# Kernel optimization log

Hardware: AMD Instinct MI355X
Metric: run time of the kernel (lower is better)

## Reference

```python
import jax, jax.numpy as jnp
import numpy as np

T, B, N = 256, 128, 64
START_IDX, END_IDX = 1, 2  # Offsets.GO, Offsets.EOS
NEG = -10000.0


def setup_inputs() -> dict:
    key = jax.random.key(0)
    k1, k2, k3 = jax.random.split(key, 3)
    unary = jax.random.normal(k1, (T, B, N), dtype=jnp.float32)          # [T, B, N] emissions
    trans = jax.random.normal(k2, (1, N, N), dtype=jnp.float32) * 0.1    # [1, N_to, N_from]
    lengths = jax.random.randint(k3, (B,), 1, T + 1)                      # 1 <= len <= T
    return {"unary": unary, "trans": trans, "lengths": lengths}


def _crf_log_partition(unary, trans, lengths):
    # unary: [T, B, N], trans: [1, N, N], lengths: [B] -> [B] log Z
    batch_size, n_tags = unary.shape[1], unary.shape[2]
    alphas0 = jnp.full((batch_size, 1, n_tags), NEG, dtype=unary.dtype)
    alphas0 = alphas0.at[:, 0, START_IDX].set(0.0)

    def step(alphas, xi):
        unary_t, i = xi  # unary_t: [B, N], i: scalar timestep
        # scores[b, to, fr] = alphas[b, 0, fr] + trans[0, to, fr] + unary_t[b, to]
        scores = alphas + trans + unary_t[:, :, None]            # [B, N, N]
        new_alphas = jax.nn.logsumexp(scores, axis=2)[:, None, :]  # [B, 1, N]
        # keep new alphas while the sequence is still active (i < length),
        # otherwise carry the old alphas forward (matches masked_fill logic).
        alphas = jnp.where((i < lengths)[:, None, None], new_alphas, alphas)
        return alphas, None

    steps = jnp.arange(unary.shape[0])
    alphas, _ = jax.lax.scan(step, alphas0, (unary, steps))
    terminal = alphas + trans[:, END_IDX]                         # [B, 1, N]
    return jax.nn.logsumexp(terminal, axis=2).squeeze(1)          # [B]


def reference(unary, trans, lengths):
    return _crf_log_partition(unary, trans, lengths)
```

## Files before the change

### kernel.cpp

```cpp
#include <hip/hip_runtime.h>

#define T_STEPS 256
#define B_SIZE  128
#define N_TAGS  64
#define BN_     8192
#define SEGS    16
#define SEGL    16
#define START_IDX 1
#define END_IDX 2

typedef float  f32x4  __attribute__((ext_vector_type(4)));
typedef float  f32x2  __attribute__((ext_vector_type(2)));
typedef short  bf16x8 __attribute__((ext_vector_type(8)));

union U8 { unsigned u[4]; bf16x8 v; };
union F4 { f32x4 v; f32x2 h[2]; float f[4]; };

__device__ __forceinline__ float fexp2(float x){float r;asm("v_exp_f32 %0, %1":"=v"(r):"v"(x));return r;}
__device__ __forceinline__ float flog2(float x){float r;asm("v_log_f32 %0, %1":"=v"(r):"v"(x));return r;}
__device__ __forceinline__ float frcp(float x){float r;asm("v_rcp_f32 %0, %1":"=v"(r):"v"(x));return r;}
__device__ __forceinline__ unsigned cvtpk(float lo,float hi){unsigned r;asm("v_cvt_pk_bf16_f32 %0, %1, %2":"=v"(r):"v"(lo),"v"(hi));return r;}
__device__ __forceinline__ void swap32(unsigned &a, unsigned &b){asm("v_permlane32_swap_b32 %0, %1":"+v"(a),"+v"(b));}
__device__ __forceinline__ void swap16(unsigned &a, unsigned &b){asm("v_permlane16_swap_b32 %0, %1":"+v"(a),"+v"(b));}
__device__ __forceinline__ f32x2 pkmul(f32x2 a, f32x2 b){f32x2 r;asm("v_pk_mul_f32 %0, %1, %2":"=v"(r):"v"(a),"v"(b));return r;}

#define MFMA16(A, B, C) __builtin_amdgcn_mfma_f32_16x16x32_bf16(A, B, C, 0, 0, 0)

__device__ __forceinline__ void wait24(){ asm volatile("s_waitcnt vmcnt(24)" ::: "memory"); __builtin_amdgcn_sched_barrier(0); }
__device__ __forceinline__ void wait16(){ asm volatile("s_waitcnt vmcnt(16)" ::: "memory"); __builtin_amdgcn_sched_barrier(0); }
__device__ __forceinline__ void wait8 (){ asm volatile("s_waitcnt vmcnt(8)"  ::: "memory"); __builtin_amdgcn_sched_barrier(0); }
__device__ __forceinline__ void wait0 (){ asm volatile("s_waitcnt vmcnt(0)"  ::: "memory"); __builtin_amdgcn_sched_barrier(0); }
__device__ __forceinline__ void wait28(){ asm volatile("s_waitcnt vmcnt(28)" ::: "memory"); __builtin_amdgcn_sched_barrier(0); }

#define IDP() do { _Pragma("unroll") \
  for (int c=0;c<2;++c) { _Pragma("unroll") \
    for (int cc=0;cc<4;++cc) { _Pragma("unroll") \
      for (int m=0;m<4;++m) { \
        int k0 = 32*c + 8*g + 2*m, n = 16*cc + col; \
        unsigned lo = (k0==n)?0x3F80u:0u, hi=(k0+1==n)?0x3F80u:0u; \
        P[c][cc].u[m] = lo | (hi<<16); } } } } while(0)

#define EVG() do { _Pragma("unroll") \
  for (int tt=0;tt<4;++tt) { _Pragma("unroll") \
    for (int r=0;r<4;++r) ev[tt][r] = __shfl(eul, 16*tt + 4*g + r, 64); } } while(0)

#define EVSCALE() do { _Pragma("unroll") \
  for (int tt=0;tt<4;++tt) { f32x2 e01,e23; \
    e01[0]=ev[tt][0]; e01[1]=ev[tt][1]; e23[0]=ev[tt][2]; e23[1]=ev[tt][3]; \
    _Pragma("unroll") for (int cc=0;cc<4;++cc) { \
      Dt[tt][cc].h[0]=pkmul(Dt[tt][cc].h[0],e01); \
      Dt[tt][cc].h[1]=pkmul(Dt[tt][cc].h[1],e23); } } } while(0)

#define RESCC() do { C += 44.361419555836498f; \
  f32x2 iv; iv[0]=5.421010862427522e-20f; iv[1]=5.421010862427522e-20f; \
  _Pragma("unroll") for (int tt=0;tt<4;++tt) { _Pragma("unroll") for (int cc=0;cc<4;++cc) { \
    Dt[tt][cc].h[0]=pkmul(Dt[tt][cc].h[0],iv); Dt[tt][cc].h[1]=pkmul(Dt[tt][cc].h[1],iv); } } } while(0)

#define CVTP() do { _Pragma("unroll") \
  for (int cc=0;cc<4;++cc) { \
    unsigned p00 = cvtpk(Dt[0][cc].f[0], Dt[0][cc].f[1]); \
    unsigned p01 = cvtpk(Dt[0][cc].f[2], Dt[0][cc].f[3]); \
    unsigned p10 = cvtpk(Dt[1][cc].f[0], Dt[1][cc].f[1]); \
    unsigned p11 = cvtpk(Dt[1][cc].f[2], Dt[1][cc].f[3]); \
    unsigned p20 = cvtpk(Dt[2][cc].f[0], Dt[2][cc].f[1]); \
    unsigned p21 = cvtpk(Dt[2][cc].f[2], Dt[2][cc].f[3]); \
    unsigned p30 = cvtpk(Dt[3][cc].f[0], Dt[3][cc].f[1]); \
    unsigned p31 = cvtpk(Dt[3][cc].f[2], Dt[3][cc].f[3]); \
    swap32(p00, p10); swap32(p01, p11); swap32(p20, p30); swap32(p21, p31); \
    swap16(p00, p10); swap16(p01, p11); swap16(p20, p30); swap16(p21, p31); \
    P[0][cc].u[0]=p00; P[0][cc].u[1]=p01; P[0][cc].u[2]=p10; P[0][cc].u[3]=p11; \
    P[1][cc].u[0]=p20; P[1][cc].u[1]=p21; P[1][cc].u[2]=p30; P[1][cc].u[3]=p31; } } while(0)

#define MFMAB() do { _Pragma("unroll") \
  for (int cc=0;cc<4;++cc) { _Pragma("unroll") \
    for (int tt=0;tt<4;++tt) { \
      f32x4 acc = MFMA16(EA[tt][0].v, P[0][cc].v, zf); \
      Dt[tt][cc].v = MFMA16(EA[tt][1].v, P[1][cc].v, acc); } } } while(0)

#define STOREP(DST) do { _Pragma("unroll") \
  for (int cc=0;cc<4;++cc) { _Pragma("unroll") \
    for (int c=0;c<2;++c) { \
      uint4 q; q.x=P[c][cc].u[0]; q.y=P[c][cc].u[1]; q.z=P[c][cc].u[2]; q.w=P[c][cc].u[3]; \
      *(uint4*)((DST) + (cc*2+c)*256) = q; } } } while(0)

__global__ __launch_bounds__(64, 2)
void crf_seg_kernel(const float* __restrict__ u, const float* __restrict__ trans,
                    const int* __restrict__ lengths,
                    unsigned* __restrict__ Mout, float* __restrict__ Cout) {
    const int bid  = blockIdx.x;
    const int b    = bid & (B_SIZE - 1);
    const int s    = bid >> 7;
    const int lane = threadIdx.x;
    const int col  = lane & 15;
    const int g    = lane >> 4;
    const float K = 1.4426950408889634f;
    const f32x4 zf = {0.f, 0.f, 0.f, 0.f};

    const int len = lengths[b];
    int n_act = len - 1 - s*SEGL;
    n_act = max(0, min(SEGL, n_act));
    unsigned* dst = Mout + (size_t)(b*SEGS + s) * 2048 + lane * 4;

    U8 P[2][4];
    if (n_act == 0) {
        IDP();
        STOREP(dst);
        if (lane == 0) Cout[b*SEGS + s] = 0.0f;
        return;
    }

    __shared__ float sT[64 * 65];
    {
#pragma unroll
        for (int k = 0; k < 64; ++k) sT[k*65 + lane] = trans[k*64 + lane];
    }
    __syncthreads();

    const bool front = (s < 8);
    U8 EA[4][2];
    if (!front) {
#pragma unroll
        for (int tt = 0; tt < 4; ++tt) {
#pragma unroll
            for (int c = 0; c < 2; ++c) {
                const float* p = &sT[(16*tt + col)*65 + 32*c + 8*g];
#pragma unroll
                for (int j2 = 0; j2 < 4; ++j2)
                    EA[tt][c].u[j2] = cvtpk(fexp2(p[2*j2]*K), fexp2(p[2*j2+1]*K));
            }
        }
    } else {
#pragma unroll
        for (int tt = 0; tt < 4; ++tt) {
#pragma unroll
            for (int c = 0; c < 2; ++c) {
#pragma unroll
                for (int j2 = 0; j2 < 4; ++j2) {
                    const int a0i = 32*c + 8*g + 2*j2;
                    EA[tt][c].u[j2] = cvtpk(fexp2(sT[a0i*65 + 16*tt + col] * K),
                                            fexp2(sT[(a0i+1)*65 + 16*tt + col] * K));
                }
            }
        }
    }

    const float* ub = u + (size_t)b * 64 + lane;
    float Ur[16];
    if (!front) {
        const int t0 = 16*s + 1;
#pragma unroll
        for (int i = 0; i < 16; ++i) Ur[i] = ub[(size_t)min(t0 + i, T_STEPS - 1) * BN_];
    } else {
        const int th = 16*s + n_act;
#pragma unroll
        for (int i = 0; i < 16; ++i) Ur[i] = ub[(size_t)max(th - i, 0) * BN_];
    }

    float C = 0.0f;
    float ev[4][4];
    F4 Dt[4][4];
    { float eul = fexp2(Ur[0] * K); EVG(); }

    if (!front) {
        IDP();
#pragma unroll 16
        for (int i = 0; i < 16; ++i) {
            if (i >= n_act) break;
            MFMAB();
            EVSCALE();
            if (i == 7) RESCC();
            CVTP();
            if (i < 15) { float eul = fexp2(Ur[i+1] * K); EVG(); }
        }
    } else {
#pragma unroll
        for (int tt = 0; tt < 4; ++tt) {
#pragma unroll
            for (int cc = 0; cc < 4; ++cc) {
#pragma unroll
                for (int r = 0; r < 4; ++r)
                    Dt[tt][cc].f[r] = (tt == cc && 4*g + r == col) ? 1.0f : 0.0f;
            }
        }
#pragma unroll 16
        for (int i = 0; i < 16; ++i) {
            if (i >= n_act) break;
            EVSCALE();
            if (i == 7) RESCC();
            CVTP();
            MFMAB();
            if (i < 15) { float eul = fexp2(Ur[i+1] * K); EVG(); }
        }
        CVTP();
    }

    STOREP(dst);
    if (lane == 0) Cout[b*SEGS + s] = C;
}

#define MLOAD(SL, SEG) do { \
    const unsigned* _mp = mbase + (size_t)(SEG) * 2048; \
    const unsigned* _mq = _mp + 1024; \
    asm volatile("global_load_dwordx4 %0, %1, off"             : "=v"(SL[0].v) : "v"(_mp)); \
    asm volatile("global_load_dwordx4 %0, %1, off offset:1024" : "=v"(SL[1].v) : "v"(_mp)); \
    asm volatile("global_load_dwordx4 %0, %1, off offset:2048" : "=v"(SL[2].v) : "v"(_mp)); \
    asm volatile("global_load_dwordx4 %0, %1, off offset:3072" : "=v"(SL[3].v) : "v"(_mp)); \
    asm volatile("global_load_dwordx4 %0, %1, off"             : "=v"(SL[4].v) : "v"(_mq)); \
    asm volatile("global_load_dwordx4 %0, %1, off offset:1024" : "=v"(SL[5].v) : "v"(_mq)); \
    asm volatile("global_load_dwordx4 %0, %1, off offset:2048" : "=v"(SL[6].v) : "v"(_mq)); \
    asm volatile("global_load_dwordx4 %0, %1, off offset:3072" : "=v"(SL[7].v) : "v"(_mq)); \
} while (0)

#define PSTEP(WN, SL, LD) do { \
    wait##WN(); \
    U8 Af0, Af1; \
    { float vs = (g < 2) ? a0 : a1; \
      float f0=__shfl(vs,sbase+0,64), f1=__shfl(vs,sbase+1,64); \
      float f2=__shfl(vs,sbase+2,64), f3=__shfl(vs,sbase+3,64); \
      float f4=__shfl(vs,sbase+4,64), f5=__shfl(vs,sbase+5,64); \
      float f6=__shfl(vs,sbase+6,64), f7=__shfl(vs,sbase+7,64); \
      Af0.u[0]=cvtpk(f0,f1); Af0.u[1]=cvtpk(f2,f3); Af0.u[2]=cvtpk(f4,f5); Af0.u[3]=cvtpk(f6,f7); } \
    { float vs = (g < 2) ? a2 : a3; \
      float f0=__shfl(vs,sbase+0,64), f1=__shfl(vs,sbase+1,64); \
      float f2=__shfl(vs,sbase+2,64), f3=__shfl(vs,sbase+3,64); \
      float f4=__shfl(vs,sbase+4,64), f5=__shfl(vs,sbase+5,64); \
      float f6=__shfl(vs,sbase+6,64), f7=__shfl(vs,sbase+7,64); \
      Af1.u[0]=cvtpk(f0,f1); Af1.u[1]=cvtpk(f2,f3); Af1.u[2]=cvtpk(f4,f5); Af1.u[3]=cvtpk(f6,f7); } \
    f32x4 q0 = MFMA16(Af0.v, SL[0].v, zf); q0 = MFMA16(Af1.v, SL[1].v, q0); \
    f32x4 q1 = MFMA16(Af0.v, SL[2].v, zf); q1 = MFMA16(Af1.v, SL[3].v, q1); \
    f32x4 q2 = MFMA16(Af0.v, SL[4].v, zf); q2 = MFMA16(Af1.v, SL[5].v, q2); \
    f32x4 q3 = MFMA16(Af0.v, SL[6].v, zf); q3 = MFMA16(Af1.v, SL[7].v, q3); \
    float n0 = q0[0], n1 = q1[0], n2 = q2[0], n3 = q3[0]; \
    float mm = fmaxf(fmaxf(n0, n1), fmaxf(n2, n3)); \
    mm = fmaxf(mm, __shfl_xor(mm, 1, 64)); mm = fmaxf(mm, __shfl_xor(mm, 2, 64)); \
    mm = fmaxf(mm, __shfl_xor(mm, 4, 64)); mm = fmaxf(mm, __shfl_xor(mm, 8, 64)); \
    float inv = frcp(mm); C2 += LN2 * flog2(mm); \
    a0 = n0 * inv; a1 = n1 * inv; a2 = n2 * inv; a3 = n3 * inv; \
    if ((LD) >= 0) { MLOAD(SL, LD); } \
} while (0)

__global__ __launch_bounds__(128, 1)
void crf_comb_kernel(const float* __restrict__ u, const float* __restrict__ trans,
                     const unsigned* __restrict__ Mbuf, const float* __restrict__ Cseg,
                     float* __restrict__ out) {
    const int tid  = threadIdx.x;
    const int wid  = tid >> 6;
    const int lane = tid & 63;
    const int col  = lane & 15;
    const int g    = lane >> 4;
    const int b    = blockIdx.x;
    const float K = 1.4426950408889634f, LN2 = 0.6931471805599453f;
    const f32x4 zf = {0.f, 0.f, 0.f, 0.f};

    __shared__ float sX[64], sY[64], sC[2];

    float a0, a1, a2, a3;
    if (wid == 0) {
        a0 = fexp2((u[(size_t)b*64 +  0 + col] + trans[( 0 + col)*64 + START_IDX]) * K);
        a1 = fexp2((u[(size_t)b*64 + 16 + col] + trans[(16 + col)*64 + START_IDX]) * K);
        a2 = fexp2((u[(size_t)b*64 + 32 + col] + trans[(32 + col)*64 + START_IDX]) * K);
        a3 = fexp2((u[(size_t)b*64 + 48 + col] + trans[(48 + col)*64 + START_IDX]) * K);
    } else {
        a0 = fexp2(trans[END_IDX*64 +  0 + col] * K);
        a1 = fexp2(trans[END_IDX*64 + 16 + col] * K);
        a2 = fexp2(trans[END_IDX*64 + 32 + col] * K);
        a3 = fexp2(trans[END_IDX*64 + 48 + col] * K);
    }

    const int sbase = (lane & 48) | ((g & 1) << 3);
    const unsigned* mbase = Mbuf + (size_t)b * SEGS * 2048 + lane * 4;

    U8 MP0[8], MP1[8], MP2[8], MP3[8];
    float C2 = 0.0f;

    if (wid == 0) {
        MLOAD(MP0, 0); MLOAD(MP1, 1); MLOAD(MP2, 2); MLOAD(MP3, 3);
        PSTEP(24, MP0,  4); PSTEP(24, MP1,  5); PSTEP(24, MP2,  6); PSTEP(24, MP3,  7);
        PSTEP(24, MP0, -1); PSTEP(16, MP1, -1); PSTEP(8,  MP2, -1); PSTEP(0,  MP3, -1);
    } else {
        MLOAD(MP0, 15); MLOAD(MP1, 14); MLOAD(MP2, 13); MLOAD(MP3, 12);
        PSTEP(24, MP0, 11); PSTEP(24, MP1, 10); PSTEP(24, MP2,  9); PSTEP(24, MP3,  8);
        PSTEP(24, MP0, -1); PSTEP(16, MP1, -1); PSTEP(8,  MP2, -1); PSTEP(0,  MP3, -1);
    }

    if (g == 0) {
        float* dstv = wid ? sY : sX;
        dstv[ 0 + col] = a0; dstv[16 + col] = a1;
        dstv[32 + col] = a2; dstv[48 + col] = a3;
    }
    if (wid == 1) {
        float cs = (lane < SEGS) ? Cseg[b*SEGS + lane] : 0.0f;
#pragma unroll
        for (int m = 1; m < 64; m <<= 1) cs += __shfl_xor(cs, m, 64);
        if (lane == 0) sC[1] = C2 + cs;
    } else if (lane == 0) sC[0] = C2;
    __syncthreads();

    if (tid < 16) {
        float part = 0.0f;
#pragma unroll
        for (int cc = 0; cc < 4; ++cc)
            part = fmaf(sX[16*cc + tid], sY[16*cc + tid], part);
        part += __shfl_xor(part, 1, 64);
        part += __shfl_xor(part, 2, 64);
        part += __shfl_xor(part, 4, 64);
        part += __shfl_xor(part, 8, 64);
        if (tid == 0) out[b] = sC[0] + sC[1] + LN2 * flog2(part);
    }
}

#define LOAD4O(RB, PTR) do { const float* _p = (PTR); \
    asm volatile("global_load_dwordx4 %0, %1, off"            : "=v"(RB[0].v) : "v"(_p)); \
    asm volatile("global_load_dwordx4 %0, %1, off offset:64"  : "=v"(RB[1].v) : "v"(_p)); \
    asm volatile("global_load_dwordx4 %0, %1, off offset:128" : "=v"(RB[2].v) : "v"(_p)); \
    asm volatile("global_load_dwordx4 %0, %1, off offset:192" : "=v"(RB[3].v) : "v"(_p)); \
} while (0)

template<bool RS, bool SNAPW>
__device__ __forceinline__ void stepfn(F4 (&D)[4], F4 (&UB)[4], const U8 (&A)[4][2],
                                       bool ccw, F4 (&wS)[4], float &snapC, float &C) {
    const float K = 1.4426950408889634f, LN2 = 0.6931471805599453f;
    const f32x4 zf = {0.f, 0.f, 0.f, 0.f};
    F4 W[4];
#pragma unroll
    for (int tt = 0; tt < 4; ++tt) {
#pragma unroll
        for (int r = 0; r < 4; ++r) W[tt].f[r] = D[tt].f[r] * fexp2(UB[tt].f[r] * K);
    }
    if (RS) {
        float m0 = fmaxf(fmaxf(W[0].f[0], W[0].f[1]), fmaxf(W[0].f[2], W[0].f[3]));
        float m1 = fmaxf(fmaxf(W[1].f[0], W[1].f[1]), fmaxf(W[1].f[2], W[1].f[3]));
        float m2 = fmaxf(fmaxf(W[2].f[0], W[2].f[1]), fmaxf(W[2].f[2], W[2].f[3]));
        float m3 = fmaxf(fmaxf(W[3].f[0], W[3].f[1]), fmaxf(W[3].f[2], W[3].f[3]));
        float mm = fmaxf(fmaxf(m0, m1), fmaxf(m2, m3));
        mm = fmaxf(mm, __shfl_xor(mm, 16, 64));
        mm = fmaxf(mm, __shfl_xor(mm, 32, 64));
        float inv = frcp(mm);
        C += LN2 * flog2(mm);
        f32x2 iv; iv[0] = inv; iv[1] = inv;
#pragma unroll
        for (int tt = 0; tt < 4; ++tt) {
            W[tt].h[0] = pkmul(W[tt].h[0], iv);
            W[tt].h[1] = pkmul(W[tt].h[1], iv);
        }
    }
    if (SNAPW) {
        if (__ballot(ccw)) {
#pragma unroll
            for (int tt = 0; tt < 4; ++tt) {
#pragma unroll
                for (int r = 0; r < 4; ++r)
                    wS[tt].f[r] = ccw ? W[tt].f[r] : wS[tt].f[r];
            }
            snapC = ccw ? C : snapC;
        }
    }
    unsigned p00 = cvtpk(W[0].f[0], W[0].f[1]), p01 = cvtpk(W[0].f[2], W[0].f[3]);
    unsigned p10 = cvtpk(W[1].f[0], W[1].f[1]), p11 = cvtpk(W[1].f[2], W[1].f[3]);
    unsigned p20 = cvtpk(W[2].f[0], W[2].f[1]), p21 = cvtpk(W[2].f[2], W[2].f[3]);
    unsigned p30 = cvtpk(W[3].f[0], W[3].f[1]), p31 = cvtpk(W[3].f[2], W[3].f[3]);
    swap32(p00, p10); swap32(p01, p11); swap32(p20, p30); swap32(p21, p31);
    swap16(p00, p10); swap16(p01, p11); swap16(p20, p30); swap16(p21, p31);
    U8 b0, b1;
    b0.u[0] = p00; b0.u[1] = p01; b0.u[2] = p10; b0.u[3] = p11;
    b1.u[0] = p20; b1.u[1] = p21; b1.u[2] = p30; b1.u[3] = p31;
#pragma unroll
    for (int tt = 0; tt < 4; ++tt) {
        f32x4 acc = MFMA16(A[tt][0].v, b0.v, zf);
        D[tt].v   = MFMA16(A[tt][1].v, b1.v, acc);
    }
}

__device__ __forceinline__ void make_frags(const float* sT, int wid, int col, int g,
                                           U8 (&A)[4][2], F4 (&D)[4]) {
    const float K = 1.4426950408889634f;
    if (wid == 0) {
#pragma unroll
        for (int tt = 0; tt < 4; ++tt) {
#pragma unroll
            for (int c = 0; c < 2; ++c) {
                const float* p = &sT[(16*tt + col)*64 + 32*c + 8*g];
#pragma unroll
                for (int j2 = 0; j2 < 4; ++j2)
                    A[tt][c].u[j2] = cvtpk(fexp2(p[2*j2]*K), fexp2(p[2*j2+1]*K));
            }
        }
#pragma unroll
        for (int tt = 0; tt < 4; ++tt) {
#pragma unroll
            for (int r = 0; r < 4; ++r)
                D[tt].f[r] = fexp2(sT[(16*tt + 4*g + r)*64 + START_IDX] * K);
        }
    } else {
#pragma unroll
        for (int tt = 0; tt < 4; ++tt) {
#pragma unroll
            for (int c = 0; c < 2; ++c) {
#pragma unroll
                for (int j2 = 0; j2 < 4; ++j2) {
                    const int a0 = 32*c + 8*g + 2*j2;
                    A[tt][c].u[j2] = cvtpk(fexp2(sT[a0*64 + 16*tt + col] * K),
                                           fexp2(sT[(a0+1)*64 + 16*tt + col] * K));
                }
            }
        }
#pragma unroll
        for (int tt = 0; tt < 4; ++tt) {
#pragma unroll
            for (int r = 0; r < 4; ++r)
                D[tt].f[r] = fexp2(sT[END_IDX*64 + 16*tt + 4*g + r] * K);
        }
    }
}

__launch_bounds__(128, 1)
__global__ void crf_fb_old(const float* __restrict__ src,
                           const float* __restrict__ trans,
                           const int* __restrict__ lengths,
                           float* __restrict__ out) {
    const int tid  = threadIdx.x;
    const int wid  = tid >> 6;
    const int lane = tid & 63;
    const int col  = lane & 15;
    const int g    = lane >> 4;
    const int bidx = blockIdx.x * 16 + col;

    __shared__ __align__(16) float sT[N_TAGS * N_TAGS];
    __shared__ __align__(16) float sW[N_TAGS * 16];
    __shared__ __align__(16) float sV[N_TAGS * 16];
    __shared__ float sCf[16], sCb[16];

    {
        const float4* t4 = (const float4*)trans;
        float4* s4 = (float4*)sT;
#pragma unroll
        for (int k2 = 0; k2 < 8; ++k2) s4[k2 * 128 + tid] = t4[k2 * 128 + tid];
    }
    __syncthreads();

    const float LN2 = 0.6931471805599453f;
    const int len = lengths[bidx];
    const int M   = (len - 1) >> 1;
    const int Kb  = (len - 1) - M;

    U8 A[4][2];
    F4 D[4];
    make_frags(sT, wid, col, g, A, D);

    int need = (wid == 0) ? (M + 1) : Kb;
    int mx = need;
#pragma unroll
    for (int m = 1; m < 64; m <<= 1) mx = max(mx, __shfl_xor(mx, m, 64));
    mx = __builtin_amdgcn_readfirstlane(mx);

    const int base = bidx * 64 + 4 * g;
    float C = 0.0f, snapC = 0.0f;
    F4 wS[4];
#pragma unroll
    for (int tt = 0; tt < 4; ++tt) wS[tt] = D[tt];

    F4 R0[4], R1[4], R2[4], R3[4], R4_[4], R5[4], R6[4], R7[4];

    if (wid == 0) {
        const float* pf = src + base;
        LOAD4O(R0, pf);            LOAD4O(R1, pf + BN_);
        LOAD4O(R2, pf + 2*BN_);    LOAD4O(R3, pf + 3*BN_);
        LOAD4O(R4_, pf + 4*BN_);   LOAD4O(R5, pf + 5*BN_);
        LOAD4O(R6, pf + 6*BN_);    LOAD4O(R7, pf + 7*BN_);
        const float* pn = pf + 8 * BN_;
        const int Nf = (mx + 7) & ~7;
        for (int s = 0; s < Nf; s += 8) {
#define FSTEP(QQ, RB, RSF) do { \
            const int t_ = s + (QQ); \
            wait28(); \
            stepfn<RSF, true>(D, RB, A, (t_ == M), wS, snapC, C); \
            LOAD4O(RB, pn); pn += BN_; \
        } while (0)
            FSTEP(0, R0, false); FSTEP(1, R1, false); FSTEP(2, R2, false);
            FSTEP(3, R3, false); FSTEP(4, R4_, false); FSTEP(5, R5, false);
            FSTEP(6, R6, false); FSTEP(7, R7, true);
#undef FSTEP
        }
        wait0();
    } else {
        const float* pb = src + base;
        {
#define PRIME(RB, q) do { int tq = max(len - 1 - (q), 0); LOAD4O(RB, pb + tq * BN_); } while (0)
            PRIME(R0, 0); PRIME(R1, 1); PRIME(R2, 2); PRIME(R3, 3);
            PRIME(R4_, 4); PRIME(R5, 5); PRIME(R6, 6); PRIME(R7, 7);
#undef PRIME
        }
        int tP = len - 9;
        const int Nb = (mx + 7) & ~7;
        for (int s = 0; s < Nb; s += 8) {
#define BSTEP(QQ, RB, RSF) do { \
            const int k_ = s + (QQ) + 1; \
            wait28(); \
            stepfn<RSF, false>(D, RB, A, false, wS, snapC, C); \
            if (__ballot(k_ == Kb)) { \
                const bool cc = (k_ == Kb); \
                _Pragma("unroll") \
                for (int tt = 0; tt < 4; ++tt) { \
                    _Pragma("unroll") \
                    for (int r = 0; r < 4; ++r) \
                        wS[tt].f[r] = cc ? D[tt].f[r] : wS[tt].f[r]; \
                } \
                snapC = cc ? C : snapC; \
            } \
            int tc = max(tP, 0); LOAD4O(RB, pb + tc * BN_); tP -= 1; \
        } while (0)
            BSTEP(0, R0, false); BSTEP(1, R1, false); BSTEP(2, R2, false);
            BSTEP(3, R3, false); BSTEP(4, R4_, false); BSTEP(5, R5, false);
            BSTEP(6, R6, false); BSTEP(7, R7, true);
#undef BSTEP
        }
        wait0();
    }

    {
        float* dstv = (wid == 0) ? sW : sV;
#pragma unroll
        for (int tt = 0; tt < 4; ++tt) {
#pragma unroll
            for (int r = 0; r < 4; ++r)
                dstv[(16*tt + 4*g + r) * 16 + col] = wS[tt].f[r];
        }
        if (g == 0) { if (wid == 0) sCf[col] = snapC; else sCb[col] = snapC; }
    }
    __syncthreads();
    if (wid == 0) {
        float part = 0.0f;
#pragma unroll
        for (int j = 0; j < 16; ++j) {
            const int n = g * 16 + j;
            part = fmaf(sW[n * 16 + col], sV[n * 16 + col], part);
        }
        part += __shfl_xor(part, 16, 64);
        part += __shfl_xor(part, 32, 64);
        if (g == 0) out[bidx] = sCf[col] + sCb[col] + LN2 * flog2(part);
    }
}

extern "C" void kernel_launch(void* const* d_in, const int* in_sizes, int n_in,
                              void* d_out, int out_size, void* d_ws, size_t ws_size,
                              hipStream_t stream) {
    const float* unary   = (const float*)d_in[0];
    const float* trans   = (const float*)d_in[1];
    const int*   lengths = (const int*)d_in[2];
    float* out = (float*)d_out;

    const size_t mcount = (size_t)B_SIZE * SEGS * 2048;
    const size_t need   = mcount * 4 + (size_t)B_SIZE * SEGS * 4;
    if (ws_size >= need) {
        unsigned* Mbuf = (unsigned*)d_ws;
        float* Cseg = (float*)((unsigned*)d_ws + mcount);
        hipLaunchKernelGGL(crf_seg_kernel, dim3(B_SIZE * SEGS), dim3(64), 0, stream,
                           unary, trans, lengths, Mbuf, Cseg);
        hipLaunchKernelGGL(crf_comb_kernel, dim3(B_SIZE), dim3(128), 0, stream,
                           unary, trans, Mbuf, Cseg, out);
    } else {
        hipLaunchKernelGGL(crf_fb_old, dim3(B_SIZE / 16), dim3(128), 0, stream,
                           unary, trans, lengths, out);
    }
}
```

Before: 33.37 us.

## Fuse segment and combine kernels using atomic last-block-done counter

Merges the per-segment transfer-matrix kernel and the combine kernel into one launch. Each 128-thread block now computes two segments (one front, one back) for a batch row, and the last of the 8 blocks per row, found through an atomic counter, performs the combine step. This removes the second kernel launch and the gap between the two kernels. In exchange it adds a hipMemsetAsync per call, a threadfence/atomic handshake, and shared-memory setup for the larger block, which may lower occupancy.

```diff
diff --git a/kernel.cpp b/kernel.cpp
--- a/kernel.cpp
+++ b/kernel.cpp
@@ -82,121 +82,6 @@
     for (int c=0;c<2;++c) { \
       uint4 q; q.x=P[c][cc].u[0]; q.y=P[c][cc].u[1]; q.z=P[c][cc].u[2]; q.w=P[c][cc].u[3]; \
       *(uint4*)((DST) + (cc*2+c)*256) = q; } } } while(0)
-
-__global__ __launch_bounds__(64, 2)
-void crf_seg_kernel(const float* __restrict__ u, const float* __restrict__ trans,
-                    const int* __restrict__ lengths,
-                    unsigned* __restrict__ Mout, float* __restrict__ Cout) {
-    const int bid  = blockIdx.x;
-    const int b    = bid & (B_SIZE - 1);
-    const int s    = bid >> 7;
-    const int lane = threadIdx.x;
-    const int col  = lane & 15;
-    const int g    = lane >> 4;
-    const float K = 1.4426950408889634f;
-    const f32x4 zf = {0.f, 0.f, 0.f, 0.f};
-
-    const int len = lengths[b];
-    int n_act = len - 1 - s*SEGL;
-    n_act = max(0, min(SEGL, n_act));
-    unsigned* dst = Mout + (size_t)(b*SEGS + s) * 2048 + lane * 4;
-
-    U8 P[2][4];
-    if (n_act == 0) {
-        IDP();
-        STOREP(dst);
-        if (lane == 0) Cout[b*SEGS + s] = 0.0f;
-        return;
-    }
-
-    __shared__ float sT[64 * 65];
-    {
-#pragma unroll
-        for (int k = 0; k < 64; ++k) sT[k*65 + lane] = trans[k*64 + lane];
-    }
-    __syncthreads();
-
-    const bool front = (s < 8);
-    U8 EA[4][2];
-    if (!front) {
-#pragma unroll
-        for (int tt = 0; tt < 4; ++tt) {
-#pragma unroll
-            for (int c = 0; c < 2; ++c) {
-                const float* p = &sT[(16*tt + col)*65 + 32*c + 8*g];
-#pragma unroll
-                for (int j2 = 0; j2 < 4; ++j2)
-                    EA[tt][c].u[j2] = cvtpk(fexp2(p[2*j2]*K), fexp2(p[2*j2+1]*K));
-            }
-        }
-    } else {
-#pragma unroll
-        for (int tt = 0; tt < 4; ++tt) {
-#pragma unroll
-            for (int c = 0; c < 2; ++c) {
-#pragma unroll
-                for (int j2 = 0; j2 < 4; ++j2) {
-                    const int a0i = 32*c + 8*g + 2*j2;
-                    EA[tt][c].u[j2] = cvtpk(fexp2(sT[a0i*65 + 16*tt + col] * K),
-                                            fexp2(sT[(a0i+1)*65 + 16*tt + col] * K));
-                }
-            }
-        }
-    }
-
-    const float* ub = u + (size_t)b * 64 + lane;
-    float Ur[16];
-    if (!front) {
-        const int t0 = 16*s + 1;
-#pragma unroll
-        for (int i = 0; i < 16; ++i) Ur[i] = ub[(size_t)min(t0 + i, T_STEPS - 1) * BN_];
-    } else {
-        const int th = 16*s + n_act;
-#pragma unroll
-        for (int i = 0; i < 16; ++i) Ur[i] = ub[(size_t)max(th - i, 0) * BN_];
-    }
-
-    float C = 0.0f;
-    float ev[4][4];
-    F4 Dt[4][4];
-    { float eul = fexp2(Ur[0] * K); EVG(); }
-
-    if (!front) {
-        IDP();
-#pragma unroll 16
-        for (int i = 0; i < 16; ++i) {
-            if (i >= n_act) break;
-            MFMAB();
-            EVSCALE();
-            if (i == 7) RESCC();
-            CVTP();
-            if (i < 15) { float eul = fexp2(Ur[i+1] * K); EVG(); }
-        }
-    } else {
-#pragma unroll
-        for (int tt = 0; tt < 4; ++tt) {
-#pragma unroll
-            for (int cc = 0; cc < 4; ++cc) {
-#pragma unroll
-                for (int r = 0; r < 4; ++r)
-                    Dt[tt][cc].f[r] = (tt == cc && 4*g + r == col) ? 1.0f : 0.0f;
-            }
-        }
-#pragma unroll 16
-        for (int i = 0; i < 16; ++i) {
-            if (i >= n_act) break;
-            EVSCALE();
-            if (i == 7) RESCC();
-            CVTP();
-            MFMAB();
-            if (i < 15) { float eul = fexp2(Ur[i+1] * K); EVG(); }
-        }
-        CVTP();
-    }
-
-    STOREP(dst);
-    if (lane == 0) Cout[b*SEGS + s] = C;
-}
 
 #define MLOAD(SL, SEG) do { \
     const unsigned* _mp = mbase + (size_t)(SEG) * 2048; \
@@ -239,61 +124,183 @@
     if ((LD) >= 0) { MLOAD(SL, LD); } \
 } while (0)
 
-__global__ __launch_bounds__(128, 1)
-void crf_comb_kernel(const float* __restrict__ u, const float* __restrict__ trans,
-                     const unsigned* __restrict__ Mbuf, const float* __restrict__ Cseg,
-                     float* __restrict__ out) {
+__global__ __launch_bounds__(128, 2)
+void crf_one(const float* __restrict__ u, const float* __restrict__ trans,
+             const int* __restrict__ lengths, unsigned* __restrict__ Mbuf,
+             float* __restrict__ Cseg, unsigned* __restrict__ cnt,
+             float* __restrict__ out) {
     const int tid  = threadIdx.x;
     const int wid  = tid >> 6;
     const int lane = tid & 63;
     const int col  = lane & 15;
     const int g    = lane >> 4;
-    const int b    = blockIdx.x;
+    const int bid  = blockIdx.x;
+    const int b    = bid & (B_SIZE - 1);
+    const int p    = bid >> 7;
     const float K = 1.4426950408889634f, LN2 = 0.6931471805599453f;
     const f32x4 zf = {0.f, 0.f, 0.f, 0.f};
 
+    __shared__ float sT[64 * 65];
     __shared__ float sX[64], sY[64], sC[2];
-
-    float a0, a1, a2, a3;
-    if (wid == 0) {
-        a0 = fexp2((u[(size_t)b*64 +  0 + col] + trans[( 0 + col)*64 + START_IDX]) * K);
-        a1 = fexp2((u[(size_t)b*64 + 16 + col] + trans[(16 + col)*64 + START_IDX]) * K);
-        a2 = fexp2((u[(size_t)b*64 + 32 + col] + trans[(32 + col)*64 + START_IDX]) * K);
-        a3 = fexp2((u[(size_t)b*64 + 48 + col] + trans[(48 + col)*64 + START_IDX]) * K);
-    } else {
-        a0 = fexp2(trans[END_IDX*64 +  0 + col] * K);
-        a1 = fexp2(trans[END_IDX*64 + 16 + col] * K);
-        a2 = fexp2(trans[END_IDX*64 + 32 + col] * K);
-        a3 = fexp2(trans[END_IDX*64 + 48 + col] * K);
-    }
-
-    const int sbase = (lane & 48) | ((g & 1) << 3);
-    const unsigned* mbase = Mbuf + (size_t)b * SEGS * 2048 + lane * 4;
-
-    U8 MP0[8], MP1[8], MP2[8], MP3[8];
-    float C2 = 0.0f;
-
-    if (wid == 0) {
-        MLOAD(MP0, 0); MLOAD(MP1, 1); MLOAD(MP2, 2); MLOAD(MP3, 3);
-        PSTEP(24, MP0,  4); PSTEP(24, MP1,  5); PSTEP(24, MP2,  6); PSTEP(24, MP3,  7);
-        PSTEP(24, MP0, -1); PSTEP(16, MP1, -1); PSTEP(8,  MP2, -1); PSTEP(0,  MP3, -1);
-    } else {
-        MLOAD(MP0, 15); MLOAD(MP1, 14); MLOAD(MP2, 13); MLOAD(MP3, 12);
-        PSTEP(24, MP0, 11); PSTEP(24, MP1, 10); PSTEP(24, MP2,  9); PSTEP(24, MP3,  8);
-        PSTEP(24, MP0, -1); PSTEP(16, MP1, -1); PSTEP(8,  MP2, -1); PSTEP(0,  MP3, -1);
-    }
-
-    if (g == 0) {
-        float* dstv = wid ? sY : sX;
-        dstv[ 0 + col] = a0; dstv[16 + col] = a1;
-        dstv[32 + col] = a2; dstv[48 + col] = a3;
-    }
-    if (wid == 1) {
-        float cs = (lane < SEGS) ? Cseg[b*SEGS + lane] : 0.0f;
-#pragma unroll
-        for (int m = 1; m < 64; m <<= 1) cs += __shfl_xor(cs, m, 64);
-        if (lane == 0) sC[1] = C2 + cs;
-    } else if (lane == 0) sC[0] = C2;
+    __shared__ int  sRet;
+
+    {
+#pragma unroll
+        for (int k = 0; k < 32; ++k) {
+            const int row = 2*k + wid;
+            sT[row*65 + lane] = trans[row*64 + lane];
+        }
+    }
+    __syncthreads();
+
+    const int len = lengths[b];
+    const int s   = (wid == 0) ? p : (8 + p);
+    const bool front = (wid == 0);
+    int n_act = len - 1 - s*SEGL;
+    n_act = max(0, min(SEGL, n_act));
+    unsigned* dst = Mbuf + (size_t)(b*SEGS + s) * 2048 + lane * 4;
+
+    {
+        U8 P[2][4];
+        float C = 0.0f;
+
+        if (n_act == 0) {
+            IDP();
+        } else {
+            U8 EA[4][2];
+            if (!front) {
+#pragma unroll
+                for (int tt = 0; tt < 4; ++tt) {
+#pragma unroll
+                    for (int c = 0; c < 2; ++c) {
+                        const float* pp = &sT[(16*tt + col)*65 + 32*c + 8*g];
+#pragma unroll
+                        for (int j2 = 0; j2 < 4; ++j2)
+                            EA[tt][c].u[j2] = cvtpk(fexp2(pp[2*j2]*K), fexp2(pp[2*j2+1]*K));
+                    }
+                }
+            } else {
+#pragma unroll
+                for (int tt = 0; tt < 4; ++tt) {
+#pragma unroll
+                    for (int c = 0; c < 2; ++c) {
+#pragma unroll
+                        for (int j2 = 0; j2 < 4; ++j2) {
+                            const int a0i = 32*c + 8*g + 2*j2;
+                            EA[tt][c].u[j2] = cvtpk(fexp2(sT[a0i*65 + 16*tt + col] * K),
+                                                    fexp2(sT[(a0i+1)*65 + 16*tt + col] * K));
+                        }
+                    }
+                }
+            }
+
+            const float* ub = u + (size_t)b * 64 + lane;
+            float Ur[16];
+            if (!front) {
+                const int t0 = 16*s + 1;
+#pragma unroll
+                for (int i = 0; i < 16; ++i) Ur[i] = ub[(size_t)min(t0 + i, T_STEPS - 1) * BN_];
+            } else {
+                const int th = 16*s + n_act;
+#pragma unroll
+                for (int i = 0; i < 16; ++i) Ur[i] = ub[(size_t)max(th - i, 0) * BN_];
+            }
+
+            float ev[4][4];
+            F4 Dt[4][4];
+            { float eul = fexp2(Ur[0] * K); EVG(); }
+
+            if (!front) {
+                IDP();
+#pragma unroll 16
+                for (int i = 0; i < 16; ++i) {
+                    if (i >= n_act) break;
+                    MFMAB();
+                    EVSCALE();
+                    if (i == 7) RESCC();
+                    CVTP();
+                    if (i < 15) { float eul = fexp2(Ur[i+1] * K); EVG(); }
+                }
+            } else {
+#pragma unroll
+                for (int tt = 0; tt < 4; ++tt) {
+#pragma unroll
+                    for (int cc = 0; cc < 4; ++cc) {
+#pragma unroll
+                        for (int r = 0; r < 4; ++r)
+                            Dt[tt][cc].f[r] = (tt == cc && 4*g + r == col) ? 1.0f : 0.0f;
+                    }
+                }
+#pragma unroll 16
+                for (int i = 0; i < 16; ++i) {
+                    if (i >= n_act) break;
+                    EVSCALE();
+                    if (i == 7) RESCC();
+                    CVTP();
+                    MFMAB();
+                    if (i < 15) { float eul = fexp2(Ur[i+1] * K); EVG(); }
+                }
+                CVTP();
+            }
+        }
+
+        STOREP(dst);
+        if (lane == 0) Cseg[b*SEGS + s] = C;
+    }
+
+    __syncthreads();
+    if (tid == 0) {
+        __threadfence();
+        unsigned old = atomicAdd(&cnt[b], 1u);
+        sRet = (old == 7u) ? 1 : 0;
+    }
+    __syncthreads();
+    if (!sRet) return;
+
+    __threadfence();
+
+    {
+        float a0, a1, a2, a3;
+        if (wid == 0) {
+            a0 = fexp2((u[(size_t)b*64 +  0 + col] + trans[( 0 + col)*64 + START_IDX]) * K);
+            a1 = fexp2((u[(size_t)b*64 + 16 + col] + trans[(16 + col)*64 + START_IDX]) * K);
+            a2 = fexp2((u[(size_t)b*64 + 32 + col] + trans[(32 + col)*64 + START_IDX]) * K);
+            a3 = fexp2((u[(size_t)b*64 + 48 + col] + trans[(48 + col)*64 + START_IDX]) * K);
+        } else {
+            a0 = fexp2(trans[END_IDX*64 +  0 + col] * K);
+            a1 = fexp2(trans[END_IDX*64 + 16 + col] * K);
+            a2 = fexp2(trans[END_IDX*64 + 32 + col] * K);
+            a3 = fexp2(trans[END_IDX*64 + 48 + col] * K);
+        }
+        const int sbase = (lane & 48) | ((g & 1) << 3);
+        const unsigned* mbase = Mbuf + (size_t)b * SEGS * 2048 + lane * 4;
+        float C2 = 0.0f;
+
+        U8 MP0[8], MP1[8], MP2[8], MP3[8];
+        if (wid == 0) {
+            MLOAD(MP0, 0); MLOAD(MP1, 1); MLOAD(MP2, 2); MLOAD(MP3, 3);
+            PSTEP(24, MP0,  4); PSTEP(24, MP1,  5); PSTEP(24, MP2,  6); PSTEP(24, MP3,  7);
+            PSTEP(24, MP0, -1); PSTEP(16, MP1, -1); PSTEP(8,  MP2, -1); PSTEP(0,  MP3, -1);
+        } else {
+            MLOAD(MP0, 15); MLOAD(MP1, 14); MLOAD(MP2, 13); MLOAD(MP3, 12);
+            PSTEP(24, MP0, 11); PSTEP(24, MP1, 10); PSTEP(24, MP2,  9); PSTEP(24, MP3,  8);
+            PSTEP(24, MP0, -1); PSTEP(16, MP1, -1); PSTEP(8,  MP2, -1); PSTEP(0,  MP3, -1);
+        }
+
+        if (g == 0) {
+            float* dstv = wid ? sY : sX;
+            dstv[ 0 + col] = a0; dstv[16 + col] = a1;
+            dstv[32 + col] = a2; dstv[48 + col] = a3;
+        }
+        if (wid == 1) {
+            float cs = (lane < SEGS) ? Cseg[b*SEGS + lane] : 0.0f;
+#pragma unroll
+            for (int m = 1; m < 64; m <<= 1) cs += __shfl_xor(cs, m, 64);
+            if (lane == 0) sC[1] = C2 + cs;
+        } else if (lane == 0) {
+            sC[0] = C2;
+        }
+    }
     __syncthreads();
 
     if (tid < 16) {
@@ -550,14 +557,15 @@
     float* out = (float*)d_out;
 
     const size_t mcount = (size_t)B_SIZE * SEGS * 2048;
-    const size_t need   = mcount * 4 + (size_t)B_SIZE * SEGS * 4;
+    const size_t csegn  = (size_t)B_SIZE * SEGS;
+    const size_t need   = mcount * 4 + csegn * 4 + B_SIZE * 4;
     if (ws_size >= need) {
         unsigned* Mbuf = (unsigned*)d_ws;
-        float* Cseg = (float*)((unsigned*)d_ws + mcount);
-        hipLaunchKernelGGL(crf_seg_kernel, dim3(B_SIZE * SEGS), dim3(64), 0, stream,
-                           unary, trans, lengths, Mbuf, Cseg);
-        hipLaunchKernelGGL(crf_comb_kernel, dim3(B_SIZE), dim3(128), 0, stream,
-                           unary, trans, Mbuf, Cseg, out);
+        float*    Cseg = (float*)(Mbuf + mcount);
+        unsigned* cnt  = (unsigned*)(Cseg + csegn);
+        hipMemsetAsync(cnt, 0, B_SIZE * sizeof(unsigned), stream);
+        hipLaunchKernelGGL(crf_one, dim3(B_SIZE * 8), dim3(128), 0, stream,
+                           unary, trans, lengths, Mbuf, Cseg, cnt, out);
     } else {
         hipLaunchKernelGGL(crf_fb_old, dim3(B_SIZE / 16), dim3(128), 0, stream,
                            unary, trans, lengths, out);
```

New measurement: 61.63 us. 84.7% more time.

## Split each segment's 64-column product across two workgroups and drop LDS staging

Applied to the files above, without the earlier changes.

The segment kernel now launches twice as many workgroups, each computing half of the column blocks (two of four) of the per-segment transfer matrix product. Each workgroup carries half the accumulator state and half the MFMA/convert work per step, which allows higher occupancy (launch bounds raised to 3 waves per SIMD). The shared-memory staging of the transition matrix and its barrier are removed in favour of direct global/vectorised reads. The cost is duplicated setup work (exp of the transition matrix, unary loads and broadcasts) in both halves, plus more uncoalesced global reads in the front path.

```diff
diff --git a/kernel.cpp b/kernel.cpp
--- a/kernel.cpp
+++ b/kernel.cpp
@@ -32,67 +32,49 @@
 __device__ __forceinline__ void wait0 (){ asm volatile("s_waitcnt vmcnt(0)"  ::: "memory"); __builtin_amdgcn_sched_barrier(0); }
 __device__ __forceinline__ void wait28(){ asm volatile("s_waitcnt vmcnt(28)" ::: "memory"); __builtin_amdgcn_sched_barrier(0); }
 
-#define IDP() do { _Pragma("unroll") \
-  for (int c=0;c<2;++c) { _Pragma("unroll") \
-    for (int cc=0;cc<4;++cc) { _Pragma("unroll") \
-      for (int m=0;m<4;++m) { \
-        int k0 = 32*c + 8*g + 2*m, n = 16*cc + col; \
-        unsigned lo = (k0==n)?0x3F80u:0u, hi=(k0+1==n)?0x3F80u:0u; \
-        P[c][cc].u[m] = lo | (hi<<16); } } } } while(0)
-
 #define EVG() do { _Pragma("unroll") \
   for (int tt=0;tt<4;++tt) { _Pragma("unroll") \
     for (int r=0;r<4;++r) ev[tt][r] = __shfl(eul, 16*tt + 4*g + r, 64); } } while(0)
 
-#define EVSCALE() do { _Pragma("unroll") \
+#define CVT2(DX, PP, J) do { \
+  unsigned p00=cvtpk(DX[0].f[0],DX[0].f[1]), p01=cvtpk(DX[0].f[2],DX[0].f[3]); \
+  unsigned p10=cvtpk(DX[1].f[0],DX[1].f[1]), p11=cvtpk(DX[1].f[2],DX[1].f[3]); \
+  unsigned p20=cvtpk(DX[2].f[0],DX[2].f[1]), p21=cvtpk(DX[2].f[2],DX[2].f[3]); \
+  unsigned p30=cvtpk(DX[3].f[0],DX[3].f[1]), p31=cvtpk(DX[3].f[2],DX[3].f[3]); \
+  swap32(p00,p10); swap32(p01,p11); swap32(p20,p30); swap32(p21,p31); \
+  swap16(p00,p10); swap16(p01,p11); swap16(p20,p30); swap16(p21,p31); \
+  PP[0][J].u[0]=p00; PP[0][J].u[1]=p01; PP[0][J].u[2]=p10; PP[0][J].u[3]=p11; \
+  PP[1][J].u[0]=p20; PP[1][J].u[1]=p21; PP[1][J].u[2]=p30; PP[1][J].u[3]=p31; } while(0)
+
+#define SCALE2() do { _Pragma("unroll") \
   for (int tt=0;tt<4;++tt) { f32x2 e01,e23; \
     e01[0]=ev[tt][0]; e01[1]=ev[tt][1]; e23[0]=ev[tt][2]; e23[1]=ev[tt][3]; \
-    _Pragma("unroll") for (int cc=0;cc<4;++cc) { \
-      Dt[tt][cc].h[0]=pkmul(Dt[tt][cc].h[0],e01); \
-      Dt[tt][cc].h[1]=pkmul(Dt[tt][cc].h[1],e23); } } } while(0)
-
-#define RESCC() do { C += 44.361419555836498f; \
-  f32x2 iv; iv[0]=5.421010862427522e-20f; iv[1]=5.421010862427522e-20f; \
-  _Pragma("unroll") for (int tt=0;tt<4;++tt) { _Pragma("unroll") for (int cc=0;cc<4;++cc) { \
-    Dt[tt][cc].h[0]=pkmul(Dt[tt][cc].h[0],iv); Dt[tt][cc].h[1]=pkmul(Dt[tt][cc].h[1],iv); } } } while(0)
-
-#define CVTP() do { _Pragma("unroll") \
-  for (int cc=0;cc<4;++cc) { \
-    unsigned p00 = cvtpk(Dt[0][cc].f[0], Dt[0][cc].f[1]); \
-    unsigned p01 = cvtpk(Dt[0][cc].f[2], Dt[0][cc].f[3]); \
-    unsigned p10 = cvtpk(Dt[1][cc].f[0], Dt[1][cc].f[1]); \
-    unsigned p11 = cvtpk(Dt[1][cc].f[2], Dt[1][cc].f[3]); \
-    unsigned p20 = cvtpk(Dt[2][cc].f[0], Dt[2][cc].f[1]); \
-    unsigned p21 = cvtpk(Dt[2][cc].f[2], Dt[2][cc].f[3]); \
-    unsigned p30 = cvtpk(Dt[3][cc].f[0], Dt[3][cc].f[1]); \
-    unsigned p31 = cvtpk(Dt[3][cc].f[2], Dt[3][cc].f[3]); \
-    swap32(p00, p10); swap32(p01, p11); swap32(p20, p30); swap32(p21, p31); \
-    swap16(p00, p10); swap16(p01, p11); swap16(p20, p30); swap16(p21, p31); \
-    P[0][cc].u[0]=p00; P[0][cc].u[1]=p01; P[0][cc].u[2]=p10; P[0][cc].u[3]=p11; \
-    P[1][cc].u[0]=p20; P[1][cc].u[1]=p21; P[1][cc].u[2]=p30; P[1][cc].u[3]=p31; } } while(0)
-
-#define MFMAB() do { _Pragma("unroll") \
-  for (int cc=0;cc<4;++cc) { _Pragma("unroll") \
-    for (int tt=0;tt<4;++tt) { \
-      f32x4 acc = MFMA16(EA[tt][0].v, P[0][cc].v, zf); \
-      Dt[tt][cc].v = MFMA16(EA[tt][1].v, P[1][cc].v, acc); } } } while(0)
-
-#define STOREP(DST) do { _Pragma("unroll") \
-  for (int cc=0;cc<4;++cc) { _Pragma("unroll") \
-    for (int c=0;c<2;++c) { \
-      uint4 q; q.x=P[c][cc].u[0]; q.y=P[c][cc].u[1]; q.z=P[c][cc].u[2]; q.w=P[c][cc].u[3]; \
-      *(uint4*)((DST) + (cc*2+c)*256) = q; } } } while(0)
-
-__global__ __launch_bounds__(64, 2)
-void crf_seg_kernel(const float* __restrict__ u, const float* __restrict__ trans,
-                    const int* __restrict__ lengths,
-                    unsigned* __restrict__ Mout, float* __restrict__ Cout) {
+    D0[tt].h[0]=pkmul(D0[tt].h[0],e01); D0[tt].h[1]=pkmul(D0[tt].h[1],e23); \
+    D1[tt].h[0]=pkmul(D1[tt].h[0],e01); D1[tt].h[1]=pkmul(D1[tt].h[1],e23); } } while(0)
+
+#define RESC2() do { f32x2 iv; iv[0]=5.421010862427522e-20f; iv[1]=iv[0]; \
+  _Pragma("unroll") for (int tt=0;tt<4;++tt) { \
+    D0[tt].h[0]=pkmul(D0[tt].h[0],iv); D0[tt].h[1]=pkmul(D0[tt].h[1],iv); \
+    D1[tt].h[0]=pkmul(D1[tt].h[0],iv); D1[tt].h[1]=pkmul(D1[tt].h[1],iv); } } while(0)
+
+#define MM2(DST, J) do { _Pragma("unroll") \
+  for (int tt=0;tt<4;++tt) { \
+    f32x4 acc_ = MFMA16(EA[tt][0].v, P[0][J].v, zf); \
+    DST[tt].v  = MFMA16(EA[tt][1].v, P[1][J].v, acc_); } } while(0)
+
+__global__ __launch_bounds__(64, 3)
+void crf_seg2(const float* __restrict__ u, const float* __restrict__ trans,
+              const int* __restrict__ lengths,
+              unsigned* __restrict__ Mout, float* __restrict__ Cout) {
     const int bid  = blockIdx.x;
     const int b    = bid & (B_SIZE - 1);
-    const int s    = bid >> 7;
+    const int q    = bid >> 7;
+    const int s    = q >> 1;
+    const int half = q & 1;
     const int lane = threadIdx.x;
     const int col  = lane & 15;
     const int g    = lane >> 4;
+    const int cb   = 2 * half;
     const float K = 1.4426950408889634f;
     const f32x4 zf = {0.f, 0.f, 0.f, 0.f};
 
@@ -101,47 +83,60 @@
     n_act = max(0, min(SEGL, n_act));
     unsigned* dst = Mout + (size_t)(b*SEGS + s) * 2048 + lane * 4;
 
-    U8 P[2][4];
+    U8 P[2][2];
+
     if (n_act == 0) {
-        IDP();
-        STOREP(dst);
-        if (lane == 0) Cout[b*SEGS + s] = 0.0f;
+#pragma unroll
+        for (int c = 0; c < 2; ++c)
+#pragma unroll
+            for (int j = 0; j < 2; ++j)
+#pragma unroll
+                for (int m = 0; m < 4; ++m) {
+                    int k0 = 32*c + 8*g + 2*m, n = 16*(cb + j) + col;
+                    unsigned lo = (k0 == n) ? 0x3F80u : 0u;
+                    unsigned hi = (k0 + 1 == n) ? 0x3F80u : 0u;
+                    P[c][j].u[m] = lo | (hi << 16);
+                }
+#pragma unroll
+        for (int j = 0; j < 2; ++j)
+#pragma unroll
+            for (int c = 0; c < 2; ++c) {
+                uint4 qd;
+                qd.x = P[c][j].u[0]; qd.y = P[c][j].u[1];
+                qd.z = P[c][j].u[2]; qd.w = P[c][j].u[3];
+                *(uint4*)(dst + ((cb + j)*2 + c) * 256) = qd;
+            }
+        if (lane == 0 && half == 0) Cout[b*SEGS + s] = 0.0f;
         return;
     }
 
-    __shared__ float sT[64 * 65];
-    {
-#pragma unroll
-        for (int k = 0; k < 64; ++k) sT[k*65 + lane] = trans[k*64 + lane];
-    }
-    __syncthreads();
-
     const bool front = (s < 8);
+
     U8 EA[4][2];
     if (!front) {
 #pragma unroll
-        for (int tt = 0; tt < 4; ++tt) {
+        for (int tt = 0; tt < 4; ++tt)
 #pragma unroll
             for (int c = 0; c < 2; ++c) {
-                const float* p = &sT[(16*tt + col)*65 + 32*c + 8*g];
-#pragma unroll
-                for (int j2 = 0; j2 < 4; ++j2)
-                    EA[tt][c].u[j2] = cvtpk(fexp2(p[2*j2]*K), fexp2(p[2*j2+1]*K));
+                const float* pp = trans + (16*tt + col)*64 + 32*c + 8*g;
+                f32x4 v0 = *(const f32x4*)pp;
+                f32x4 v1 = *(const f32x4*)(pp + 4);
+                EA[tt][c].u[0] = cvtpk(fexp2(v0[0]*K), fexp2(v0[1]*K));
+                EA[tt][c].u[1] = cvtpk(fexp2(v0[2]*K), fexp2(v0[3]*K));
+                EA[tt][c].u[2] = cvtpk(fexp2(v1[0]*K), fexp2(v1[1]*K));
+                EA[tt][c].u[3] = cvtpk(fexp2(v1[2]*K), fexp2(v1[3]*K));
             }
-        }
-    } else {
-#pragma unroll
-        for (int tt = 0; tt < 4; ++tt) {
-#pragma unroll
-            for (int c = 0; c < 2; ++c) {
+    } else {
+#pragma unroll
+        for (int tt = 0; tt < 4; ++tt)
+#pragma unroll
+            for (int c = 0; c < 2; ++c)
 #pragma unroll
                 for (int j2 = 0; j2 < 4; ++j2) {
-                    const int a0i = 32*c + 8*g + 2*j2;
-                    EA[tt][c].u[j2] = cvtpk(fexp2(sT[a0i*65 + 16*tt + col] * K),
-                                            fexp2(sT[(a0i+1)*65 + 16*tt + col] * K));
+                    const int a0 = 32*c + 8*g + 2*j2;
+                    EA[tt][c].u[j2] = cvtpk(fexp2(trans[a0*64 + 16*tt + col] * K),
+                                            fexp2(trans[(a0+1)*64 + 16*tt + col] * K));
                 }
-            }
-        }
     }
 
     const float* ub = u + (size_t)b * 64 + lane;
@@ -158,44 +153,65 @@
 
     float C = 0.0f;
     float ev[4][4];
-    F4 Dt[4][4];
+    F4 D0[4], D1[4];
     { float eul = fexp2(Ur[0] * K); EVG(); }
 
     if (!front) {
-        IDP();
+#pragma unroll
+        for (int c = 0; c < 2; ++c)
+#pragma unroll
+            for (int j = 0; j < 2; ++j)
+#pragma unroll
+                for (int m = 0; m < 4; ++m) {
+                    int k0 = 32*c + 8*g + 2*m, n = 16*(cb + j) + col;
+                    unsigned lo = (k0 == n) ? 0x3F80u : 0u;
+                    unsigned hi = (k0 + 1 == n) ? 0x3F80u : 0u;
+                    P[c][j].u[m] = lo | (hi << 16);
+                }
 #pragma unroll 16
         for (int i = 0; i < 16; ++i) {
             if (i >= n_act) break;
-            MFMAB();
-            EVSCALE();
-            if (i == 7) RESCC();
-            CVTP();
+            MM2(D0, 0);
+            MM2(D1, 1);
+            SCALE2();
+            if (i == 7) { C += 44.361419555836498f; RESC2(); }
+            CVT2(D0, P, 0);
+            CVT2(D1, P, 1);
             if (i < 15) { float eul = fexp2(Ur[i+1] * K); EVG(); }
         }
     } else {
 #pragma unroll
-        for (int tt = 0; tt < 4; ++tt) {
-#pragma unroll
-            for (int cc = 0; cc < 4; ++cc) {
-#pragma unroll
-                for (int r = 0; r < 4; ++r)
-                    Dt[tt][cc].f[r] = (tt == cc && 4*g + r == col) ? 1.0f : 0.0f;
+        for (int tt = 0; tt < 4; ++tt)
+#pragma unroll
+            for (int r = 0; r < 4; ++r) {
+                D0[tt].f[r] = (tt == cb     && 4*g + r == col) ? 1.0f : 0.0f;
+                D1[tt].f[r] = (tt == cb + 1 && 4*g + r == col) ? 1.0f : 0.0f;
             }
-        }
 #pragma unroll 16
         for (int i = 0; i < 16; ++i) {
             if (i >= n_act) break;
-            EVSCALE();
-            if (i == 7) RESCC();
-            CVTP();
-            MFMAB();
+            SCALE2();
+            if (i == 7) { C += 44.361419555836498f; RESC2(); }
+            CVT2(D0, P, 0);
+            CVT2(D1, P, 1);
+            MM2(D0, 0);
+            MM2(D1, 1);
             if (i < 15) { float eul = fexp2(Ur[i+1] * K); EVG(); }
         }
-        CVTP();
-    }
-
-    STOREP(dst);
-    if (lane == 0) Cout[b*SEGS + s] = C;
+        CVT2(D0, P, 0);
+        CVT2(D1, P, 1);
+    }
+
+#pragma unroll
+    for (int j = 0; j < 2; ++j)
+#pragma unroll
+        for (int c = 0; c < 2; ++c) {
+            uint4 qd;
+            qd.x = P[c][j].u[0]; qd.y = P[c][j].u[1];
+            qd.z = P[c][j].u[2]; qd.w = P[c][j].u[3];
+            *(uint4*)(dst + ((cb + j)*2 + c) * 256) = qd;
+        }
+    if (lane == 0 && half == 0) Cout[b*SEGS + s] = C;
 }
 
 #define MLOAD(SL, SEG) do { \
@@ -485,7 +501,7 @@
     } else {
         const float* pb = src + base;
         {
-#define PRIME(RB, q) do { int tq = max(len - 1 - (q), 0); LOAD4O(RB, pb + tq * BN_); } while (0)
+#define PRIME(RB, qq) do { int tq = max(len - 1 - (qq), 0); LOAD4O(RB, pb + tq * BN_); } while (0)
             PRIME(R0, 0); PRIME(R1, 1); PRIME(R2, 2); PRIME(R3, 3);
             PRIME(R4_, 4); PRIME(R5, 5); PRIME(R6, 6); PRIME(R7, 7);
 #undef PRIME
@@ -554,7 +570,7 @@
     if (ws_size >= need) {
         unsigned* Mbuf = (unsigned*)d_ws;
         float* Cseg = (float*)((unsigned*)d_ws + mcount);
-        hipLaunchKernelGGL(crf_seg_kernel, dim3(B_SIZE * SEGS), dim3(64), 0, stream,
+        hipLaunchKernelGGL(crf_seg2, dim3(B_SIZE * 32), dim3(64), 0, stream,
                            unary, trans, lengths, Mbuf, Cseg);
         hipLaunchKernelGGL(crf_comb_kernel, dim3(B_SIZE), dim3(128), 0, stream,
                            unary, trans, Mbuf, Cseg, out);
```

New measurement: 34.19 us. +2.5%, slower.
